# Optimization experiments

Hardware: AMD Instinct MI355X
Metric: run time of the kernel (lower is better)

## Reference

```python
import jax, jax.numpy as jnp
import numpy as np

N_NODES = 50000
N_EDGES = 1000000
F_IN, HID, N_CLS, HEADS = 128, 16, 40, 8
NEG_SLOPE = 0.2


def setup_inputs() -> dict:
    key = jax.random.key(0)
    ks = jax.random.split(key, 12)
    x = jax.random.normal(ks[0], (N_NODES, F_IN), dtype=jnp.float32)
    edge_index = jax.random.randint(ks[1], (2, N_EDGES), 0, N_NODES, dtype=jnp.int32)
    s1 = 1.0 / np.sqrt(F_IN)
    s2 = 1.0 / np.sqrt(HID)
    return {
        "x": x,
        "edge_index": edge_index,
        # conv1: heads=8, out=HID, concat=False (mean over heads)
        "W1": jax.random.normal(ks[2], (F_IN, HEADS * HID), dtype=jnp.float32) * s1,
        "att_src1": jax.random.normal(ks[3], (HEADS, HID), dtype=jnp.float32) * s2,
        "att_dst1": jax.random.normal(ks[4], (HEADS, HID), dtype=jnp.float32) * s2,
        "b1": jnp.zeros((HID,), dtype=jnp.float32),
        # conv2: heads=1, out=N_CLS
        "W2": jax.random.normal(ks[5], (HID, N_CLS), dtype=jnp.float32) * s2,
        "att_src2": jax.random.normal(ks[6], (1, N_CLS), dtype=jnp.float32),
        "att_dst2": jax.random.normal(ks[7], (1, N_CLS), dtype=jnp.float32),
        "b2": jnp.zeros((N_CLS,), dtype=jnp.float32),
    }


def _gat_conv(x, src, dst, W, att_src, att_dst, num_nodes):
    """One GATConv (PyG semantics, eval mode). Returns [N, H, C]."""
    H, C = att_src.shape
    h = (x @ W).reshape(-1, H, C)                       # [N, H, C]
    a_s = (h * att_src[None]).sum(-1)                   # [N, H]
    a_d = (h * att_dst[None]).sum(-1)                   # [N, H]
    e = jax.nn.leaky_relu(a_s[src] + a_d[dst], NEG_SLOPE)  # [E, H]
    # segment softmax over edges grouped by destination node
    m = jax.ops.segment_max(e, dst, num_segments=num_nodes)     # [N, H]
    ex = jnp.exp(e - m[dst])
    denom = jax.ops.segment_sum(ex, dst, num_segments=num_nodes)
    alpha = ex / (denom[dst] + 1e-16)                   # [E, H]
    msg = h[src] * alpha[:, :, None]                    # [E, H, C]
    return jax.ops.segment_sum(msg, dst, num_segments=num_nodes)  # [N, H, C]


def reference(x, edge_index, W1, att_src1, att_dst1, b1, W2, att_src2, att_dst2, b2):
    n = x.shape[0]
    loops = jnp.arange(n, dtype=edge_index.dtype)
    src = jnp.concatenate([edge_index[0], loops])
    dst = jnp.concatenate([edge_index[1], loops])

    # conv1: concat=False -> mean over heads, then bias; then ELU
    h1 = _gat_conv(x, src, dst, W1, att_src1, att_dst1, n).mean(axis=1) + b1
    h1 = jax.nn.elu(h1)
    # dropout is identity in eval mode

    # conv2: heads=1, concat (trivial) -> squeeze head dim, add bias
    h2 = _gat_conv(h1, src, dst, W2, att_src2, att_dst2, n)[:, 0, :] + b2
    return jax.nn.log_softmax(h2, axis=1)
```

## Files before the change

### kernel.cpp

```cpp
#include <hip/hip_runtime.h>
#include <hip/hip_fp16.h>
#include <math.h>

#define N_NODES 50000
#define N_EDGES 1000000
#define F_IN 128
#define HID 16
#define N_CLS 40
#define HEADS 8
#define ET (N_EDGES + N_NODES)
#define XB ((N_NODES + 63) / 64)
#define HB ((ET + 255) / 256)
#define NSCB ((N_NODES + 255) / 256)

typedef __attribute__((ext_vector_type(8))) _Float16 f16x8;
typedef __attribute__((ext_vector_type(4))) float f32x4;

__device__ __forceinline__ unsigned encf(float f) {
  unsigned b = __float_as_uint(f);
  return (b & 0x80000000u) ? ~b : (b | 0x80000000u);
}
__device__ __forceinline__ float decf(unsigned k) {
  unsigned b = (k & 0x80000000u) ? (k ^ 0x80000000u) : ~k;
  return __uint_as_float(b);
}


__global__ __launch_bounds__(256) void k_xform1(
    const float* __restrict__ x, const float* __restrict__ W1,
    const float* __restrict__ att_s, const float* __restrict__ att_d,
    const int* __restrict__ ei, int* __restrict__ deg, int* __restrict__ epos,
    __half* __restrict__ h1, float* __restrict__ as1, float* __restrict__ ad1,
    unsigned* __restrict__ enc1) {
  if (blockIdx.x >= XB) {
    int i = (blockIdx.x - XB) * 256 + threadIdx.x;
    if (i < ET) {
      int dd = (i < N_EDGES) ? ei[N_EDGES + i] : (i - N_EDGES);
      epos[i] = atomicAdd(&deg[dd], 1);
    }
    return;
  }
  __shared__ __half xl[64 * 128];
  __shared__ __half wt[128 * 128];
  __shared__ unsigned encl[8];
  int t = threadIdx.x;
  if (t < 8) encl[t] = 0u;
  int base = blockIdx.x * 64;
  const float4* x4 = (const float4*)x;
  const float4* W4 = (const float4*)W1;

#pragma unroll
  for (int u = 0; u < 8; u++) {
    int i = t + u * 256;
    int n = i >> 5, q = i & 31;
    int gn = base + n;
    float4 v = {0.f, 0.f, 0.f, 0.f};
    if (gn < N_NODES) v = x4[(size_t)gn * 32 + q];
    uint2 pk;
    __half2* ph = (__half2*)&pk;
    ph[0] = __floats2half2_rn(v.x, v.y);
    ph[1] = __floats2half2_rn(v.z, v.w);
    unsigned byte = (unsigned)(n * 256 + q * 8) ^ ((n & 7) << 4);
    *(uint2*)((char*)xl + byte) = pk;
  }
#pragma unroll
  for (int u = 0; u < 4; u++) {
    int i = t + u * 256;
    int kt = i >> 5, ct = i & 31;
    int k0 = kt * 4;
    float4 r0 = W4[(size_t)(k0 + 0) * 32 + ct];
    float4 r1 = W4[(size_t)(k0 + 1) * 32 + ct];
    float4 r2 = W4[(size_t)(k0 + 2) * 32 + ct];
    float4 r3 = W4[(size_t)(k0 + 3) * 32 + ct];
    int chb = ct * 4;
    uint2 pk;
    __half2* ph = (__half2*)&pk;
    ph[0] = __floats2half2_rn(r0.x, r1.x); ph[1] = __floats2half2_rn(r2.x, r3.x);
    *(uint2*)((char*)wt + (((unsigned)((chb + 0) * 256 + k0 * 2)) ^ (((chb + 0) & 7) << 4))) = pk;
    ph[0] = __floats2half2_rn(r0.y, r1.y); ph[1] = __floats2half2_rn(r2.y, r3.y);
    *(uint2*)((char*)wt + (((unsigned)((chb + 1) * 256 + k0 * 2)) ^ (((chb + 1) & 7) << 4))) = pk;
    ph[0] = __floats2half2_rn(r0.z, r1.z); ph[1] = __floats2half2_rn(r2.z, r3.z);
    *(uint2*)((char*)wt + (((unsigned)((chb + 2) * 256 + k0 * 2)) ^ (((chb + 2) & 7) << 4))) = pk;
    ph[0] = __floats2half2_rn(r0.w, r1.w); ph[1] = __floats2half2_rn(r2.w, r3.w);
    *(uint2*)((char*)wt + (((unsigned)((chb + 3) * 256 + k0 * 2)) ^ (((chb + 3) & 7) << 4))) = pk;
  }
  __syncthreads();

  int l = t & 63, wv = t >> 6;
  int lm = l & 15, lh = l >> 4;
  int n0 = wv * 16;
  int node = n0 + lm;
  bool wvalid = (base + n0) < N_NODES;

  f32x4 acc[8];
#pragma unroll
  for (int f = 0; f < 8; f++) acc[f] = (f32x4){0.f, 0.f, 0.f, 0.f};

#pragma unroll
  for (int kb = 0; kb < 4; kb++) {
    int kbase = kb * 32 + lh * 8;
    unsigned ab = ((unsigned)(node * 256 + kbase * 2)) ^ ((node & 7) << 4);
    f16x8 af = *(const f16x8*)((const char*)xl + ab);
#pragma unroll
    for (int f = 0; f < 8; f++) {
      int ch = f * 16 + lm;
      unsigned bb = ((unsigned)(ch * 256 + kbase * 2)) ^ ((ch & 7) << 4);
      f16x8 bf = *(const f16x8*)((const char*)wt + bb);
      acc[f] = __builtin_amdgcn_mfma_f32_16x16x32_f16(af, bf, acc[f], 0, 0, 0);
    }
  }

  int nr = base + n0 + lh * 4;
#pragma unroll
  for (int f = 0; f < 8; f++) {
    float asv = att_s[f * 16 + lm];
    float adv = att_d[f * 16 + lm];
    float ps0 = acc[f].x * asv, ps1 = acc[f].y * asv;
    float ps2 = acc[f].z * asv, ps3 = acc[f].w * asv;
    float pd0 = acc[f].x * adv, pd1 = acc[f].y * adv;
    float pd2 = acc[f].z * adv, pd3 = acc[f].w * adv;
#pragma unroll
    for (int off = 1; off <= 8; off <<= 1) {
      ps0 += __shfl_xor(ps0, off); ps1 += __shfl_xor(ps1, off);
      ps2 += __shfl_xor(ps2, off); ps3 += __shfl_xor(ps3, off);
      pd0 += __shfl_xor(pd0, off); pd1 += __shfl_xor(pd1, off);
      pd2 += __shfl_xor(pd2, off); pd3 += __shfl_xor(pd3, off);
    }
    if (wvalid) {
      if (lm == 0) {
        as1[(nr + 0) * 8 + f] = ps0; ad1[(nr + 0) * 8 + f] = pd0;
        as1[(nr + 1) * 8 + f] = ps1; ad1[(nr + 1) * 8 + f] = pd1;
        as1[(nr + 2) * 8 + f] = ps2; ad1[(nr + 2) * 8 + f] = pd2;
        as1[(nr + 3) * 8 + f] = ps3; ad1[(nr + 3) * 8 + f] = pd3;
        float m = fmaxf(fmaxf(ps0, ps1), fmaxf(ps2, ps3));
        atomicMax(&encl[f], encf(m));
      }
      int cb = f * 16 + lm;
      h1[(size_t)(nr + 0) * 128 + cb] = __float2half(acc[f].x);
      h1[(size_t)(nr + 1) * 128 + cb] = __float2half(acc[f].y);
      h1[(size_t)(nr + 2) * 128 + cb] = __float2half(acc[f].z);
      h1[(size_t)(nr + 3) * 128 + cb] = __float2half(acc[f].w);
    }
  }
  __syncthreads();
  if (t < 8) atomicMax(&enc1[t], encl[t]);
}


__global__ __launch_bounds__(256) void k_scanA(const int* __restrict__ deg,
                                               int* __restrict__ bsum) {
  int i = blockIdx.x * 256 + threadIdx.x;
  int v = (i < N_NODES) ? deg[i] : 0;
#pragma unroll
  for (int off = 32; off; off >>= 1) v += __shfl_xor(v, off);
  __shared__ int ws[4];
  if ((threadIdx.x & 63) == 0) ws[threadIdx.x >> 6] = v;
  __syncthreads();
  if (threadIdx.x == 0) bsum[blockIdx.x] = ws[0] + ws[1] + ws[2] + ws[3];
}

__global__ __launch_bounds__(256) void k_scanB(const int* __restrict__ bsum,
                                               int* __restrict__ boff,
                                               int* __restrict__ start,
                                               const unsigned* __restrict__ enc1,
                                               float* __restrict__ fmax1) {
  __shared__ int s[256];
  int t = threadIdx.x;
  int v0 = (t < NSCB) ? bsum[t] : 0;
  s[t] = v0;
  __syncthreads();
  for (int off = 1; off < 256; off <<= 1) {
    int v = (t >= off) ? s[t - off] : 0;
    __syncthreads();
    s[t] += v;
    __syncthreads();
  }
  boff[t] = s[t] - v0;
  if (t == 0) start[N_NODES] = ET;
  if (t < 8) fmax1[t] = decf(enc1[t]);
}

__global__ __launch_bounds__(256) void k_scanC(const int* __restrict__ deg,
                                               const int* __restrict__ boff,
                                               int* __restrict__ start) {
  __shared__ int s[256];
  int t = threadIdx.x;
  int i = blockIdx.x * 256 + t;
  int v0 = (i < N_NODES) ? deg[i] : 0;
  s[t] = v0;
  __syncthreads();
  for (int off = 1; off < 256; off <<= 1) {
    int v = (t >= off) ? s[t - off] : 0;
    __syncthreads();
    s[t] += v;
    __syncthreads();
  }
  if (i < N_NODES) start[i] = boff[blockIdx.x] + s[t] - v0;
}

__global__ void k_scatter(const int* __restrict__ ei, const int* __restrict__ start,
                          const int* __restrict__ epos, int* __restrict__ esrc) {
  int i = blockIdx.x * blockDim.x + threadIdx.x;
  if (i >= ET) return;
  int s, d;
  if (i < N_EDGES) { s = ei[i]; d = ei[N_EDGES + i]; }
  else { s = i - N_EDGES; d = s; }
  esrc[start[d] + epos[i]] = s;
}


__global__ __launch_bounds__(256) void k_agg1(
    const __half* __restrict__ h1, const float* __restrict__ as1,
    const float* __restrict__ ad1, const int* __restrict__ start,
    const int* __restrict__ esrc, const float* __restrict__ b1,
    const float* __restrict__ W2, const float* __restrict__ att_s2,
    const float* __restrict__ att_d2, const float* __restrict__ fmax1,
    __half* __restrict__ h2, float* __restrict__ as2, float* __restrict__ ad2) {
  __shared__ __align__(16) __half2 p_t[4][4 * 164];
  __shared__ __align__(16) int s_off[4][4][20];
  __shared__ float w2s[16 * 40];
  int t = threadIdx.x;
  for (int i = t; i < 640; i += 256) w2s[i] = W2[i];
  __syncthreads();

  int wave = t >> 6, lane = t & 63;
  int g = lane >> 4, li = lane & 15;
  int d = blockIdx.x * 16 + wave * 4 + g;
  int s0 = start[d];
  int deg = start[d + 1] - s0;

  int dm = deg;
  dm = max(dm, __shfl_xor(dm, 16));
  dm = max(dm, __shfl_xor(dm, 32));

  float4 av0 = *(const float4*)(ad1 + d * 8);
  float4 av1 = *(const float4*)(ad1 + d * 8 + 4);
  float ad_[8] = {av0.x, av0.y, av0.z, av0.w, av1.x, av1.y, av1.z, av1.w};
  float c_[8];
#pragma unroll
  for (int h = 0; h < 8; h++) {
    float e = fmax1[h] + ad_[h];
    c_[h] = e > 0.f ? e : 0.2f * e;
  }

  float den = 0.f;
  float accf[8];
#pragma unroll
  for (int k = 0; k < 8; k++) accf[k] = 0.f;

  int hsel = li >> 1;
  const char* h1l = (const char*)(h1 + li * 8);
  __half2* ptw = &p_t[wave][g * 164];
  const int* so = &s_off[wave][g][0];

  for (int be = 0; be < dm; be += 16) {
    int cnt = deg - be;
    bool act = li < cnt;
    int s = 0;
    if (act) s = esrc[s0 + be + li];
    s_off[wave][g][li] = act ? (s << 8) : 0;
    float4 p0 = {0.f, 0.f, 0.f, 0.f}, p1 = {0.f, 0.f, 0.f, 0.f};
    if (act) {
      p0 = *(const float4*)(as1 + (size_t)s * 8);
      p1 = *(const float4*)(as1 + (size_t)s * 8 + 4);
    }
    float ev[8] = {p0.x, p0.y, p0.z, p0.w, p1.x, p1.y, p1.z, p1.w};
#pragma unroll
    for (int h = 0; h < 8; h++) {
      float v = ev[h] + ad_[h];
      v = v > 0.f ? v : 0.2f * v;
      float pv = act ? __expf(v - c_[h]) : 0.f;
      __half hp = __float2half(pv);
      ptw[h * 20 + li] = __half2{hp, hp};
    }
    asm volatile("s_waitcnt lgkmcnt(0)" ::: "memory");

    int cm = min(dm - be, 16);
    const __half2* pt = ptw + hsel * 20;
    __half2 a0 = __floats2half2_rn(0.f, 0.f);
    __half2 a1 = __floats2half2_rn(0.f, 0.f);
    __half2 a2 = __floats2half2_rn(0.f, 0.f);
    __half2 a3 = __floats2half2_rn(0.f, 0.f);
    for (int e = 0; e < cm; e += 8) {
      int4 s4 = *(const int4*)&so[e];
      int4 s8 = *(const int4*)&so[e + 4];
      uint4 pwA = *(const uint4*)&pt[e];
      uint4 pwB = *(const uint4*)&pt[e + 4];
      const __half2* ppA = (const __half2*)&pwA;
      const __half2* ppB = (const __half2*)&pwB;
      uint4 hA = *(const uint4*)(h1l + (unsigned)s4.x);
      uint4 hB = *(const uint4*)(h1l + (unsigned)s4.y);
      uint4 hC = *(const uint4*)(h1l + (unsigned)s4.z);
      uint4 hD = *(const uint4*)(h1l + (unsigned)s4.w);
      uint4 hE = *(const uint4*)(h1l + (unsigned)s8.x);
      uint4 hF = *(const uint4*)(h1l + (unsigned)s8.y);
      uint4 hG = *(const uint4*)(h1l + (unsigned)s8.z);
      uint4 hH = *(const uint4*)(h1l + (unsigned)s8.w);
      const __half2* vA = (const __half2*)&hA;
      const __half2* vB = (const __half2*)&hB;
      const __half2* vC = (const __half2*)&hC;
      const __half2* vD = (const __half2*)&hD;
      const __half2* vE = (const __half2*)&hE;
      const __half2* vF = (const __half2*)&hF;
      const __half2* vG = (const __half2*)&hG;
      const __half2* vH = (const __half2*)&hH;
      a0 = __hfma2(vA[0], ppA[0], a0); a1 = __hfma2(vA[1], ppA[0], a1);
      a2 = __hfma2(vA[2], ppA[0], a2); a3 = __hfma2(vA[3], ppA[0], a3);
      a0 = __hfma2(vB[0], ppA[1], a0); a1 = __hfma2(vB[1], ppA[1], a1);
      a2 = __hfma2(vB[2], ppA[1], a2); a3 = __hfma2(vB[3], ppA[1], a3);
      a0 = __hfma2(vC[0], ppA[2], a0); a1 = __hfma2(vC[1], ppA[2], a1);
      a2 = __hfma2(vC[2], ppA[2], a2); a3 = __hfma2(vC[3], ppA[2], a3);
      a0 = __hfma2(vD[0], ppA[3], a0); a1 = __hfma2(vD[1], ppA[3], a1);
      a2 = __hfma2(vD[2], ppA[3], a2); a3 = __hfma2(vD[3], ppA[3], a3);
      a0 = __hfma2(vE[0], ppB[0], a0); a1 = __hfma2(vE[1], ppB[0], a1);
      a2 = __hfma2(vE[2], ppB[0], a2); a3 = __hfma2(vE[3], ppB[0], a3);
      a0 = __hfma2(vF[0], ppB[1], a0); a1 = __hfma2(vF[1], ppB[1], a1);
      a2 = __hfma2(vF[2], ppB[1], a2); a3 = __hfma2(vF[3], ppB[1], a3);
      a0 = __hfma2(vG[0], ppB[2], a0); a1 = __hfma2(vG[1], ppB[2], a1);
      a2 = __hfma2(vG[2], ppB[2], a2); a3 = __hfma2(vG[3], ppB[2], a3);
      a0 = __hfma2(vH[0], ppB[3], a0); a1 = __hfma2(vH[1], ppB[3], a1);
      a2 = __hfma2(vH[2], ppB[3], a2); a3 = __hfma2(vH[3], ppB[3], a3);
      den += __low2float(ppA[0]) + __low2float(ppA[1]) +
             __low2float(ppA[2]) + __low2float(ppA[3]) +
             __low2float(ppB[0]) + __low2float(ppB[1]) +
             __low2float(ppB[2]) + __low2float(ppB[3]);
    }
    float2 f0 = __half22float2(a0), f1 = __half22float2(a1);
    float2 f2 = __half22float2(a2), f3 = __half22float2(a3);
    accf[0] += f0.x; accf[1] += f0.y; accf[2] += f1.x; accf[3] += f1.y;
    accf[4] += f2.x; accf[5] += f2.y; accf[6] += f3.x; accf[7] += f3.y;
    asm volatile("s_waitcnt lgkmcnt(0)" ::: "memory");
  }

  float sc = 0.125f / den;
#pragma unroll
  for (int k = 0; k < 8; k++) accf[k] *= sc;
#pragma unroll
  for (int off = 2; off <= 8; off <<= 1) {
#pragma unroll
    for (int k = 0; k < 8; k++) accf[k] += __shfl_xor(accf[k], off);
  }
  int jb = (li & 1) * 8;
  float4 b1a = *(const float4*)(b1 + jb);
  float4 b1b = *(const float4*)(b1 + jb + 4);
  float bv[8] = {b1a.x, b1a.y, b1a.z, b1a.w, b1b.x, b1b.y, b1b.z, b1b.w};
  float r[8];
#pragma unroll
  for (int k = 0; k < 8; k++) {
    float v = accf[k] + bv[k];
    r[k] = v > 0.f ? v : __expf(v) - 1.f;
  }
  float ro[8];
#pragma unroll
  for (int k = 0; k < 8; k++) ro[k] = __shfl_xor(r[k], 1);

  float o0 = 0.f, o1 = 0.f, o2 = 0.f;
  bool has2 = li < 8;
#pragma unroll
  for (int k = 0; k < 16; k++) {
    float rk;
    if (k < 8) rk = (li & 1) ? ro[k] : r[k];
    else       rk = (li & 1) ? r[k - 8] : ro[k - 8];
    o0 = fmaf(rk, w2s[k * 40 + li], o0);
    o1 = fmaf(rk, w2s[k * 40 + li + 16], o1);
    if (has2) o2 = fmaf(rk, w2s[k * 40 + li + 32], o2);
  }
  __half* h2r = h2 + d * 40;
  h2r[li] = __float2half(o0);
  h2r[li + 16] = __float2half(o1);
  if (has2) h2r[li + 32] = __float2half(o2);

  float sv = o0 * att_s2[li] + o1 * att_s2[li + 16];
  float dv = o0 * att_d2[li] + o1 * att_d2[li + 16];
  if (has2) {
    sv = fmaf(o2, att_s2[li + 32], sv);
    dv = fmaf(o2, att_d2[li + 32], dv);
  }
#pragma unroll
  for (int off = 1; off <= 8; off <<= 1) {
    sv += __shfl_xor(sv, off);
    dv += __shfl_xor(dv, off);
  }
  if (li == 0) { as2[d] = sv; ad2[d] = dv; }
}


__global__ __launch_bounds__(256) void k_maxas2(const float* __restrict__ as2,
                                                unsigned* __restrict__ enc) {
  int t = blockIdx.x * 256 + threadIdx.x;
  float mx = -1e30f;
  for (int r = t; r < N_NODES; r += 16384) mx = fmaxf(mx, as2[r]);
#pragma unroll
  for (int off = 32; off; off >>= 1) mx = fmaxf(mx, __shfl_xor(mx, off));
  if ((threadIdx.x & 63) == 0) atomicMax(enc, encf(mx));
}


__global__ __launch_bounds__(256) void k_agg2(
    const __half* __restrict__ h2, const float* __restrict__ as2,
    const float* __restrict__ ad2, const int* __restrict__ start,
    const int* __restrict__ esrc, const float* __restrict__ b2,
    const unsigned* __restrict__ as2maxEnc, float* __restrict__ out) {
  __shared__ __align__(16) float p_l[4][64];
  __shared__ __align__(16) int s_l[4][64];
  int wave = threadIdx.x >> 6, lane = threadIdx.x & 63;
  int d = blockIdx.x * 4 + wave;
  if (d >= N_NODES) return;
  int s0 = start[d];
  int deg = start[d + 1] - s0;
  float adv = ad2[d];
  float cm = decf(as2maxEnc[0]) + adv;
  cm = cm > 0.f ? cm : 0.2f * cm;

  int cp = lane % 20;
  int es = lane / 20;
  const char* h2b = (const char*)h2 + cp * 4;

  float den = 0.f, acc0 = 0.f, acc1 = 0.f;
  for (int be = 0; be < deg; be += 64) {
    int cnt = min(64, deg - be);
    if (lane < cnt) {
      int s = esrc[s0 + be + lane];
      s_l[wave][lane] = s * 80;
      float e = as2[s] + adv;
      e = e > 0.f ? e : 0.2f * e;
      float p = __expf(e - cm);
      den += p;
      p_l[wave][lane] = p;
    }
    asm volatile("s_waitcnt lgkmcnt(0)" ::: "memory");
    if (es < 3) {
      int i = 0;
      for (; i + 5 < cnt; i += 6) {
        int eA = i + es, eB = i + 3 + es;
        int sbA = s_l[wave][eA], sbB = s_l[wave][eB];
        float pA = p_l[wave][eA], pB = p_l[wave][eB];
        __half2 hvA = *(const __half2*)(h2b + (unsigned)sbA);
        __half2 hvB = *(const __half2*)(h2b + (unsigned)sbB);
        acc0 = fmaf(__half2float(hvA.x), pA, acc0);
        acc1 = fmaf(__half2float(hvA.y), pA, acc1);
        acc0 = fmaf(__half2float(hvB.x), pB, acc0);
        acc1 = fmaf(__half2float(hvB.y), pB, acc1);
      }
      for (; i < cnt; i += 3) {
        int e = i + es;
        if (e < cnt) {
          int sb = s_l[wave][e];
          float p = p_l[wave][e];
          __half2 hv = *(const __half2*)(h2b + (unsigned)sb);
          acc0 = fmaf(__half2float(hv.x), p, acc0);
          acc1 = fmaf(__half2float(hv.y), p, acc1);
        }
      }
    }
    asm volatile("s_waitcnt lgkmcnt(0)" ::: "memory");
  }
#pragma unroll
  for (int off = 32; off; off >>= 1) den += __shfl_xor(den, off);
  float iv = 1.f / den;

  acc0 += __shfl(acc0, lane + 20) + __shfl(acc0, lane + 40);
  acc1 += __shfl(acc1, lane + 20) + __shfl(acc1, lane + 40);
  float va = __shfl(acc0, lane >> 1);
  float vb = __shfl(acc1, lane >> 1);
  float v = (lane & 1) ? vb : va;
  v = (lane < N_CLS) ? v * iv + b2[lane] : -1e30f;

  float mx = v;
#pragma unroll
  for (int off = 32; off; off >>= 1) mx = fmaxf(mx, __shfl_xor(mx, off));
  float ex = (lane < N_CLS) ? __expf(v - mx) : 0.f;
  float sm = ex;
#pragma unroll
  for (int off = 32; off; off >>= 1) sm += __shfl_xor(sm, off);
  float lse = logf(sm);
  if (lane < N_CLS) out[d * N_CLS + lane] = (v - mx) - lse;
}


extern "C" void kernel_launch(void* const* d_in, const int* in_sizes, int n_in,
                              void* d_out, int out_size, void* d_ws, size_t ws_size,
                              hipStream_t stream) {
  const float* x    = (const float*)d_in[0];
  const int*   ei   = (const int*)d_in[1];
  const float* W1   = (const float*)d_in[2];
  const float* as1w = (const float*)d_in[3];
  const float* ad1w = (const float*)d_in[4];
  const float* b1   = (const float*)d_in[5];
  const float* W2   = (const float*)d_in[6];
  const float* as2w = (const float*)d_in[7];
  const float* ad2w = (const float*)d_in[8];
  const float* b2   = (const float*)d_in[9];
  float* out = (float*)d_out;

  char* ws = (char*)d_ws;
  size_t off = 0;
  auto alloc = [&](size_t bytes) -> void* {
    void* p = ws + off;
    off += (bytes + 255) & ~(size_t)255;
    return p;
  };
  __half* h1   = (__half*)alloc((size_t)N_NODES * 128 * 2);
  float* as1   = (float*)alloc((size_t)N_NODES * 8 * 4);
  float* ad1   = (float*)alloc((size_t)N_NODES * 8 * 4);
  __half* h2   = (__half*)alloc((size_t)N_NODES * 40 * 2);
  float* as2   = (float*)alloc((size_t)N_NODES * 4);
  float* ad2   = (float*)alloc((size_t)N_NODES * 4);
  size_t zbytes = (size_t)N_NODES * 4 + 256;
  int* deg     = (int*)alloc(zbytes);
  unsigned* maxenc = (unsigned*)(deg + N_NODES);
  int* start   = (int*)alloc((size_t)(N_NODES + 1) * 4);
  int* esrc    = (int*)alloc((size_t)ET * 4);
  int* epos    = (int*)alloc((size_t)ET * 4);
  int* bsum    = (int*)alloc((size_t)NSCB * 4);
  int* boff    = (int*)alloc(256 * 4);
  float* fmax1 = (float*)alloc(32);

  (void)hipMemsetAsync(deg, 0, zbytes, stream);

  k_xform1<<<XB + HB, 256, 0, stream>>>(x, W1, as1w, ad1w, ei, deg, epos,
                                        h1, as1, ad1, maxenc);
  k_scanA<<<NSCB, 256, 0, stream>>>(deg, bsum);
  k_scanB<<<1, 256, 0, stream>>>(bsum, boff, start, maxenc, fmax1);
  k_scanC<<<NSCB, 256, 0, stream>>>(deg, boff, start);
  k_scatter<<<HB, 256, 0, stream>>>(ei, start, epos, esrc);

  k_agg1<<<N_NODES / 16, 256, 0, stream>>>(h1, as1, ad1, start, esrc, b1,
                                           W2, as2w, ad2w, fmax1,
                                           h2, as2, ad2);
  k_maxas2<<<64, 256, 0, stream>>>(as2, maxenc + 8);
  k_agg2<<<(N_NODES + 3) / 4, 256, 0, stream>>>(h2, as2, ad2, start, esrc, b2,
                                                maxenc + 8, out);
}
```

Baseline: 186.9 us.

## Pretranspose W1 to fp16 once and stage h1 stores through shared memory

```diff
diff --git a/kernel.cpp b/kernel.cpp
--- a/kernel.cpp
+++ b/kernel.cpp
@@ -26,8 +26,16 @@
 }
 
 
+__global__ __launch_bounds__(256) void k_wprep(const float* __restrict__ W1,
+                                               __half* __restrict__ wt16) {
+  int i = blockIdx.x * 256 + threadIdx.x;
+  int ch = i >> 7, k = i & 127;
+  wt16[ch * 128 + k] = __float2half(W1[(size_t)k * 128 + ch]);
+}
+
+
 __global__ __launch_bounds__(256) void k_xform1(
-    const float* __restrict__ x, const float* __restrict__ W1,
+    const float* __restrict__ x, const __half* __restrict__ wt16,
     const float* __restrict__ att_s, const float* __restrict__ att_d,
     const int* __restrict__ ei, int* __restrict__ deg, int* __restrict__ epos,
     __half* __restrict__ h1, float* __restrict__ as1, float* __restrict__ ad1,
@@ -47,7 +55,6 @@
   if (t < 8) encl[t] = 0u;
   int base = blockIdx.x * 64;
   const float4* x4 = (const float4*)x;
-  const float4* W4 = (const float4*)W1;
 
 #pragma unroll
   for (int u = 0; u < 8; u++) {
@@ -63,26 +70,16 @@
     unsigned byte = (unsigned)(n * 256 + q * 8) ^ ((n & 7) << 4);
     *(uint2*)((char*)xl + byte) = pk;
   }
-#pragma unroll
-  for (int u = 0; u < 4; u++) {
-    int i = t + u * 256;
-    int kt = i >> 5, ct = i & 31;
-    int k0 = kt * 4;
-    float4 r0 = W4[(size_t)(k0 + 0) * 32 + ct];
-    float4 r1 = W4[(size_t)(k0 + 1) * 32 + ct];
-    float4 r2 = W4[(size_t)(k0 + 2) * 32 + ct];
-    float4 r3 = W4[(size_t)(k0 + 3) * 32 + ct];
-    int chb = ct * 4;
-    uint2 pk;
-    __half2* ph = (__half2*)&pk;
-    ph[0] = __floats2half2_rn(r0.x, r1.x); ph[1] = __floats2half2_rn(r2.x, r3.x);
-    *(uint2*)((char*)wt + (((unsigned)((chb + 0) * 256 + k0 * 2)) ^ (((chb + 0) & 7) << 4))) = pk;
-    ph[0] = __floats2half2_rn(r0.y, r1.y); ph[1] = __floats2half2_rn(r2.y, r3.y);
-    *(uint2*)((char*)wt + (((unsigned)((chb + 1) * 256 + k0 * 2)) ^ (((chb + 1) & 7) << 4))) = pk;
-    ph[0] = __floats2half2_rn(r0.z, r1.z); ph[1] = __floats2half2_rn(r2.z, r3.z);
-    *(uint2*)((char*)wt + (((unsigned)((chb + 2) * 256 + k0 * 2)) ^ (((chb + 2) & 7) << 4))) = pk;
-    ph[0] = __floats2half2_rn(r0.w, r1.w); ph[1] = __floats2half2_rn(r2.w, r3.w);
-    *(uint2*)((char*)wt + (((unsigned)((chb + 3) * 256 + k0 * 2)) ^ (((chb + 3) & 7) << 4))) = pk;
+  {
+    const uint4* wt4 = (const uint4*)wt16;
+#pragma unroll
+    for (int u = 0; u < 8; u++) {
+      int i = t + u * 256;
+      unsigned lin = (unsigned)i * 16;
+      unsigned row = lin >> 8;
+      unsigned byte = lin ^ ((row & 7) << 4);
+      *(uint4*)((char*)wt + byte) = wt4[i];
+    }
   }
   __syncthreads();
 
@@ -110,7 +107,8 @@
     }
   }
 
-  int nr = base + n0 + lh * 4;
+  int nr_loc = n0 + lh * 4;
+  int nr = base + nr_loc;
 #pragma unroll
   for (int f = 0; f < 8; f++) {
     float asv = att_s[f * 16 + lm];
@@ -126,23 +124,36 @@
       pd0 += __shfl_xor(pd0, off); pd1 += __shfl_xor(pd1, off);
       pd2 += __shfl_xor(pd2, off); pd3 += __shfl_xor(pd3, off);
     }
-    if (wvalid) {
-      if (lm == 0) {
-        as1[(nr + 0) * 8 + f] = ps0; ad1[(nr + 0) * 8 + f] = pd0;
-        as1[(nr + 1) * 8 + f] = ps1; ad1[(nr + 1) * 8 + f] = pd1;
-        as1[(nr + 2) * 8 + f] = ps2; ad1[(nr + 2) * 8 + f] = pd2;
-        as1[(nr + 3) * 8 + f] = ps3; ad1[(nr + 3) * 8 + f] = pd3;
-        float m = fmaxf(fmaxf(ps0, ps1), fmaxf(ps2, ps3));
-        atomicMax(&encl[f], encf(m));
-      }
-      int cb = f * 16 + lm;
-      h1[(size_t)(nr + 0) * 128 + cb] = __float2half(acc[f].x);
-      h1[(size_t)(nr + 1) * 128 + cb] = __float2half(acc[f].y);
-      h1[(size_t)(nr + 2) * 128 + cb] = __float2half(acc[f].z);
-      h1[(size_t)(nr + 3) * 128 + cb] = __float2half(acc[f].w);
-    }
-  }
-  __syncthreads();
+    if (wvalid && lm == 0) {
+      as1[(nr + 0) * 8 + f] = ps0; ad1[(nr + 0) * 8 + f] = pd0;
+      as1[(nr + 1) * 8 + f] = ps1; ad1[(nr + 1) * 8 + f] = pd1;
+      as1[(nr + 2) * 8 + f] = ps2; ad1[(nr + 2) * 8 + f] = pd2;
+      as1[(nr + 3) * 8 + f] = ps3; ad1[(nr + 3) * 8 + f] = pd3;
+      float m = fmaxf(fmaxf(ps0, ps1), fmaxf(ps2, ps3));
+      atomicMax(&encl[f], encf(m));
+    }
+  }
+
+  __syncthreads();
+#pragma unroll
+  for (int f = 0; f < 8; f++) {
+    int cb = f * 16 + lm;
+    xl[(nr_loc + 0) * 128 + cb] = __float2half(acc[f].x);
+    xl[(nr_loc + 1) * 128 + cb] = __float2half(acc[f].y);
+    xl[(nr_loc + 2) * 128 + cb] = __float2half(acc[f].z);
+    xl[(nr_loc + 3) * 128 + cb] = __float2half(acc[f].w);
+  }
+  __syncthreads();
+  {
+    const uint4* src = (const uint4*)xl;
+    uint4* dst = (uint4*)(h1 + (size_t)base * 128);
+#pragma unroll
+    for (int u = 0; u < 4; u++) {
+      int i = t + u * 256;
+      int nl = i >> 4;
+      if (base + nl < N_NODES) dst[i] = src[i];
+    }
+  }
   if (t < 8) atomicMax(&enc1[t], encl[t]);
 }
 
@@ -506,6 +517,7 @@
   __half* h2   = (__half*)alloc((size_t)N_NODES * 40 * 2);
   float* as2   = (float*)alloc((size_t)N_NODES * 4);
   float* ad2   = (float*)alloc((size_t)N_NODES * 4);
+  __half* wt16 = (__half*)alloc((size_t)128 * 128 * 2);
   size_t zbytes = (size_t)N_NODES * 4 + 256;
   int* deg     = (int*)alloc(zbytes);
   unsigned* maxenc = (unsigned*)(deg + N_NODES);
@@ -518,7 +530,8 @@
 
   (void)hipMemsetAsync(deg, 0, zbytes, stream);
 
-  k_xform1<<<XB + HB, 256, 0, stream>>>(x, W1, as1w, ad1w, ei, deg, epos,
+  k_wprep<<<64, 256, 0, stream>>>(W1, wt16);
+  k_xform1<<<XB + HB, 256, 0, stream>>>(x, wt16, as1w, ad1w, ei, deg, epos,
                                         h1, as1, ad1, maxenc);
   k_scanA<<<NSCB, 256, 0, stream>>>(deg, bsum);
   k_scanB<<<1, 256, 0, stream>>>(bsum, boff, start, maxenc, fmax1);
```

Result: no change. 188.0 us (+0.6%).
